# Kernel tuning notes

Hardware: AMD Instinct MI355X
Metric: run time of the kernel (lower is better)

The kernel has to match this reference:

```python
import jax, jax.numpy as jnp
import numpy as np

B, KA, KT, KX = 512, 8, 32, 512
DA, DS, A = 256, 768, 32


def setup_inputs() -> dict:
    key = jax.random.key(0)
    ks = jax.random.split(key, 16)
    inp = {
        'author_emb': jax.random.normal(ks[0], (B, KA, DA), jnp.float32),
        'title_emb': jax.random.normal(ks[1], (B, KT, DS), jnp.float32),
        'text_emb': jax.random.normal(ks[2], (B, KX, DS), jnp.float32),
        # attention params (fc: Linear(emb_dim, 32), context: (1,32))
        'Wa': jax.random.normal(ks[3], (A, DA), jnp.float32) / np.sqrt(DA),
        'ba': jnp.zeros((A,), jnp.float32),
        'ca': jax.random.normal(ks[4], (1, A), jnp.float32),
        'Wt': jax.random.normal(ks[5], (A, DS), jnp.float32) / np.sqrt(DS),
        'bt': jnp.zeros((A,), jnp.float32),
        'ct': jax.random.normal(ks[6], (1, A), jnp.float32),
        'Wx': jax.random.normal(ks[7], (A, DS), jnp.float32) / np.sqrt(DS),
        'bx': jnp.zeros((A,), jnp.float32),
        'cx': jax.random.normal(ks[8], (1, A), jnp.float32),
        # scoring heads Linear(dim, 1)
        'Wfa': jax.random.normal(ks[9], (1, DA), jnp.float32) / np.sqrt(DA),
        'bfa': jnp.zeros((1,), jnp.float32),
        'Wft': jax.random.normal(ks[10], (1, DS), jnp.float32) / np.sqrt(DS),
        'bft': jnp.zeros((1,), jnp.float32),
        'Wfx': jax.random.normal(ks[11], (1, DS), jnp.float32) / np.sqrt(DS),
        'bfx': jnp.zeros((1,), jnp.float32),
        # classifier Linear(3, 2)
        'Wc': jax.random.normal(ks[12], (2, 3), jnp.float32) / np.sqrt(3.0),
        'bc': jnp.zeros((2,), jnp.float32),
    }
    return inp


def _attn_pool(X, W, b, ctx):
    # X: [B,K,D]; fc+tanh: [B,K,A]
    o = jnp.tanh(jnp.einsum('bkd,ad->bka', X, W) + b)
    s = jnp.einsum('a,bka->bk', ctx[0], o)  # context @ o.T per sample
    # torch does F.softmax(o, dim=0) on a (1,K) tensor: softmax over the
    # singleton dim -> all-ones weights (faithful reproduction of source).
    w = jax.nn.softmax(s[:, None, :], axis=1)[:, 0, :]  # [B,K], == ones
    return jnp.einsum('bk,bkd->bd', w, X)  # [B,D]


def reference(author_emb, title_emb, text_emb,
              Wa, ba, ca, Wt, bt, ct, Wx, bx, cx,
              Wfa, bfa, Wft, bft, Wfx, bfx, Wc, bc):
    pa = _attn_pool(author_emb, Wa, ba, ca)  # [B,DA]
    pt = _attn_pool(title_emb, Wt, bt, ct)   # [B,DS]
    px = _attn_pool(text_emb, Wx, bx, cx)    # [B,DS]
    sa = pa @ Wfa.T + bfa  # [B,1]
    st = pt @ Wft.T + bft
    sx = px @ Wfx.T + bfx
    score = jax.nn.sigmoid(jnp.concatenate([sa, st, sx], axis=1))  # [B,3]
    logits = score @ Wc.T + bc  # [B,2]
    return jax.nn.softmax(logits, axis=1)
```

## Files before the change

kernel.cpp:

```cpp
#include <hip/hip_runtime.h>
#include <math.h>

#define BATCH 512
#define KA 8
#define KT 32
#define KX 512
#define DA 256
#define DS 768

#define AUTHOR_F4 (KA * DA / 4)
#define TITLE_F4  (KT * DS / 4)
#define TEXT_F4   (KX * DS / 4)
#define WA_F4 (DA / 4)
#define WS_F4 (DS / 4)

#define NT 512
#define NWAVE (NT / 64)

__global__ __launch_bounds__(NT) void fd_fused_kernel(
    const float* __restrict__ author,
    const float* __restrict__ title,
    const float* __restrict__ text,
    const float* __restrict__ Wfa,
    const float* __restrict__ bfa,
    const float* __restrict__ Wft,
    const float* __restrict__ bft,
    const float* __restrict__ Wfx,
    const float* __restrict__ bfx,
    const float* __restrict__ Wc,
    const float* __restrict__ bc,
    float* __restrict__ out)
{
    __shared__ float4 s_wfa[WA_F4];
    __shared__ float4 s_wft[WS_F4];
    __shared__ float4 s_wfx[WS_F4];
    __shared__ float s_red[3][NWAVE];

    const int t = threadIdx.x;
    const int b = blockIdx.x;

    if (t < WA_F4) s_wfa[t] = ((const float4*)Wfa)[t];
    if (t < WS_F4) {
        s_wft[t] = ((const float4*)Wft)[t];
        s_wfx[t] = ((const float4*)Wfx)[t];
    }
    __syncthreads();

    const float4* tx = (const float4*)(text  + (size_t)b * (KX * DS));
    const float4* tt = (const float4*)(title + (size_t)b * (KT * DS));
    const float4* ta = (const float4*)(author + (size_t)b * (KA * DA));

    float accx = 0.f, acct = 0.f, acca = 0.f;

    {
        int d4 = t % WS_F4;
        const int step = NT % WS_F4;
        #pragma unroll 4
        for (int i = t; i < TEXT_F4; i += NT) {
            float4 v = tx[i];
            float4 w = s_wfx[d4];
            accx += v.x * w.x + v.y * w.y + v.z * w.z + v.w * w.w;
            d4 += step; if (d4 >= WS_F4) d4 -= WS_F4;
        }
    }
    {
        int d4 = t % WS_F4;
        const int step = NT % WS_F4;
        #pragma unroll
        for (int i = t; i < TITLE_F4; i += NT) {
            float4 v = tt[i];
            float4 w = s_wft[d4];
            acct += v.x * w.x + v.y * w.y + v.z * w.z + v.w * w.w;
            d4 += step; if (d4 >= WS_F4) d4 -= WS_F4;
        }
    }
    {
        float4 v = ta[t];
        float4 w = s_wfa[t % WA_F4];
        acca += v.x * w.x + v.y * w.y + v.z * w.z + v.w * w.w;
    }

    #pragma unroll
    for (int off = 32; off > 0; off >>= 1) {
        accx += __shfl_down(accx, off, 64);
        acct += __shfl_down(acct, off, 64);
        acca += __shfl_down(acca, off, 64);
    }
    const int wave = t >> 6;
    const int lane = t & 63;
    if (lane == 0) {
        s_red[0][wave] = accx;
        s_red[1][wave] = acct;
        s_red[2][wave] = acca;
    }
    __syncthreads();

    if (t == 0) {
        float SX = 0.f, ST = 0.f, SA = 0.f;
        #pragma unroll
        for (int w = 0; w < NWAVE; ++w) {
            SX += s_red[0][w];
            ST += s_red[1][w];
            SA += s_red[2][w];
        }
        float va = SA + bfa[0];
        float vt = ST + bft[0];
        float vx = SX + bfx[0];
        float s0 = 1.f / (1.f + expf(-va));
        float s1 = 1.f / (1.f + expf(-vt));
        float s2 = 1.f / (1.f + expf(-vx));
        float l0 = Wc[0] * s0 + Wc[1] * s1 + Wc[2] * s2 + bc[0];
        float l1 = Wc[3] * s0 + Wc[4] * s1 + Wc[5] * s2 + bc[1];
        float m = fmaxf(l0, l1);
        float e0 = expf(l0 - m), e1 = expf(l1 - m);
        float inv = 1.f / (e0 + e1);
        out[2 * b + 0] = e0 * inv;
        out[2 * b + 1] = e1 * inv;
    }
}

extern "C" void kernel_launch(void* const* d_in, const int* in_sizes, int n_in,
                              void* d_out, int out_size, void* d_ws, size_t ws_size,
                              hipStream_t stream) {
    const float* author = (const float*)d_in[0];
    const float* title  = (const float*)d_in[1];
    const float* text   = (const float*)d_in[2];
    const float* Wfa = (const float*)d_in[12];
    const float* bfa = (const float*)d_in[13];
    const float* Wft = (const float*)d_in[14];
    const float* bft = (const float*)d_in[15];
    const float* Wfx = (const float*)d_in[16];
    const float* bfx = (const float*)d_in[17];
    const float* Wc  = (const float*)d_in[18];
    const float* bc  = (const float*)d_in[19];
    float* out = (float*)d_out;

    fd_fused_kernel<<<BATCH, NT, 0, stream>>>(
        author, title, text, Wfa, bfa, Wft, bft, Wfx, bfx, Wc, bc, out);
}
```

Before: 151.0 us.

## Use 1024-thread blocks with register-held weights and three-way split accumulators

Doubles the block size to 1024 threads. Because 1024 mod 192 is 64, each thread only ever touches three fixed weight float4s, so the scoring-head weights are loaded straight into registers and the shared-memory staging and its barrier are removed. The text and title loops are unrolled in groups of three with separate accumulators to raise memory-level parallelism, and the author load is guarded for the larger block. The kernel streams hundreds of MB of text embeddings and is likely already near HBM bandwidth, so the gain may be small; the launch-bounds hint may also constrain registers.

```diff
diff --git a/kernel.cpp b/kernel.cpp
--- a/kernel.cpp
+++ b/kernel.cpp
@@ -8,16 +8,17 @@
 #define DA 256
 #define DS 768
 
-#define AUTHOR_F4 (KA * DA / 4)
 #define TITLE_F4  (KT * DS / 4)
 #define TEXT_F4   (KX * DS / 4)
 #define WA_F4 (DA / 4)
 #define WS_F4 (DS / 4)
 
-#define NT 512
+#define NT 1024
 #define NWAVE (NT / 64)
+#define TEXT_ITER  (TEXT_F4 / NT)
+#define TITLE_ITER (TITLE_F4 / NT)
 
-__global__ __launch_bounds__(NT) void fd_fused_kernel(
+__global__ __launch_bounds__(NT, 8) void fd_fused_kernel(
     const float* __restrict__ author,
     const float* __restrict__ title,
     const float* __restrict__ text,
@@ -31,53 +32,56 @@
     const float* __restrict__ bc,
     float* __restrict__ out)
 {
-    __shared__ float4 s_wfa[WA_F4];
-    __shared__ float4 s_wft[WS_F4];
-    __shared__ float4 s_wfx[WS_F4];
     __shared__ float s_red[3][NWAVE];
 
     const int t = threadIdx.x;
     const int b = blockIdx.x;
 
-    if (t < WA_F4) s_wfa[t] = ((const float4*)Wfa)[t];
-    if (t < WS_F4) {
-        s_wft[t] = ((const float4*)Wft)[t];
-        s_wfx[t] = ((const float4*)Wfx)[t];
-    }
-    __syncthreads();
+    const int d0 = t % WS_F4;
+    const int d1 = (d0 + 64) % WS_F4;
+    const int d2 = (d0 + 128) % WS_F4;
 
-    const float4* tx = (const float4*)(text  + (size_t)b * (KX * DS));
-    const float4* tt = (const float4*)(title + (size_t)b * (KT * DS));
-    const float4* ta = (const float4*)(author + (size_t)b * (KA * DA));
+    const float4* wxp = (const float4*)Wfx;
+    const float4* wtp = (const float4*)Wft;
 
-    float accx = 0.f, acct = 0.f, acca = 0.f;
-
+    float ax0 = 0.f, ax1 = 0.f, ax2 = 0.f;
     {
-        int d4 = t % WS_F4;
-        const int step = NT % WS_F4;
-        #pragma unroll 4
-        for (int i = t; i < TEXT_F4; i += NT) {
-            float4 v = tx[i];
-            float4 w = s_wfx[d4];
-            accx += v.x * w.x + v.y * w.y + v.z * w.z + v.w * w.w;
-            d4 += step; if (d4 >= WS_F4) d4 -= WS_F4;
+        const float4 w0 = wxp[d0], w1 = wxp[d1], w2 = wxp[d2];
+        const float4* bx = (const float4*)(text + (size_t)b * (KX * DS)) + t;
+        #pragma unroll 2
+        for (int j = 0; j < TEXT_ITER; j += 3) {
+            float4 v0 = bx[(j + 0) * NT];
+            float4 v1 = bx[(j + 1) * NT];
+            float4 v2 = bx[(j + 2) * NT];
+            ax0 += v0.x * w0.x + v0.y * w0.y + v0.z * w0.z + v0.w * w0.w;
+            ax1 += v1.x * w1.x + v1.y * w1.y + v1.z * w1.z + v1.w * w1.w;
+            ax2 += v2.x * w2.x + v2.y * w2.y + v2.z * w2.z + v2.w * w2.w;
         }
     }
+    float accx = ax0 + ax1 + ax2;
+
+    float acct;
     {
-        int d4 = t % WS_F4;
-        const int step = NT % WS_F4;
+        const float4 w0 = wtp[d0], w1 = wtp[d1], w2 = wtp[d2];
+        const float4* bt = (const float4*)(title + (size_t)b * (KT * DS)) + t;
+        float at0 = 0.f, at1 = 0.f, at2 = 0.f;
         #pragma unroll
-        for (int i = t; i < TITLE_F4; i += NT) {
-            float4 v = tt[i];
-            float4 w = s_wft[d4];
-            acct += v.x * w.x + v.y * w.y + v.z * w.z + v.w * w.w;
-            d4 += step; if (d4 >= WS_F4) d4 -= WS_F4;
+        for (int j = 0; j < TITLE_ITER; j += 3) {
+            float4 v0 = bt[(j + 0) * NT];
+            float4 v1 = bt[(j + 1) * NT];
+            float4 v2 = bt[(j + 2) * NT];
+            at0 += v0.x * w0.x + v0.y * w0.y + v0.z * w0.z + v0.w * w0.w;
+            at1 += v1.x * w1.x + v1.y * w1.y + v1.z * w1.z + v1.w * w1.w;
+            at2 += v2.x * w2.x + v2.y * w2.y + v2.z * w2.z + v2.w * w2.w;
         }
+        acct = at0 + at1 + at2;
     }
-    {
-        float4 v = ta[t];
-        float4 w = s_wfa[t % WA_F4];
-        acca += v.x * w.x + v.y * w.y + v.z * w.z + v.w * w.w;
+
+    float acca = 0.f;
+    if (t < KA * DA / 4) {
+        float4 v = ((const float4*)(author + (size_t)b * (KA * DA)))[t];
+        float4 w = ((const float4*)Wfa)[t % WA_F4];
+        acca = v.x * w.x + v.y * w.y + v.z * w.z + v.w * w.w;
     }
 
     #pragma unroll
```

Result: no change. 149.4 us (-1.1%).
